# Performance work log

Measured on AMD Instinct MI355X. Metric: run time of the kernel, lower is better.

The kernel has to match this reference:

```python
import jax, jax.numpy as jnp
import numpy as np

B, S, DM, H, DK, DV, CUT = 2, 256, 512, 8, 64, 64, 16
LN_EPS = 1e-5


def get_con_vecs(seq, cutoff):
    # seq: (B, H, S, d). Faithful to torch: raw row-major reshape, NOT a transpose.
    b, h, s, d = seq.shape
    D = h * d
    flat = seq.reshape(b, s, D)                       # raw reinterpretation as in torch
    t = jnp.broadcast_to(flat[:, None], (b, s, s, D)) # (B, S_rep, S_orig, D)
    t = t.transpose(0, 3, 1, 2)                       # (B, D, S, S)
    up = jnp.triu(t)
    up = jnp.flip(up, axis=2)
    up = jnp.pad(up, ((0, 0), (0, 0), (1, 0), (0, 0)))[:, :, :-1, :]
    low = jnp.tril(t)
    low = jnp.flip(low, axis=2)
    mtx = jnp.concatenate([up, low], axis=-1)         # (B, D, S, 2S)
    mtx = mtx.transpose(0, 2, 3, 1)                   # (B, S, 2S, D)
    mtx = mtx.reshape(b, h, s, 2 * s, d)              # raw reinterpretation as in torch
    c = min(cutoff, s)
    return mtx[:, :, :, s - c:s + c, :]               # (B, H, S, 2c, d)


def setup_inputs():
    key = jax.random.key(0)
    ks = jax.random.split(key, 14)
    n = lambda k, shp, sc=0.02: jax.random.normal(k, shp, dtype=jnp.float32) * sc
    return {
        "Q": jax.random.normal(ks[0], (B, S, DM), dtype=jnp.float32),
        "K": jax.random.normal(ks[1], (B, S, DM), dtype=jnp.float32),
        "V": jax.random.normal(ks[2], (B, S, DM), dtype=jnp.float32),
        "attn_mask": jax.random.randint(ks[3], (B, S, S), 0, 2).astype(bool),
        "WQ": n(ks[4], (DM, H * DK)), "bQ": jnp.zeros((H * DK,), jnp.float32),
        "WK": n(ks[5], (DM, H * DK)), "bK": jnp.zeros((H * DK,), jnp.float32),
        "WV": n(ks[6], (DM, H * DV)), "bV": jnp.zeros((H * DV,), jnp.float32),
        "Wo": n(ks[7], (H * DV, DM)), "bo": jnp.zeros((DM,), jnp.float32),
        "gamma": jnp.ones((DM,), jnp.float32), "beta": jnp.zeros((DM,), jnp.float32),
    }


def reference(Q, K, V, attn_mask, WQ, bQ, WK, bK, WV, bV, Wo, bo, gamma, beta):
    b = Q.shape[0]
    q_s = (Q @ WQ + bQ).reshape(b, -1, H, DK).transpose(0, 2, 1, 3)  # (B,H,S,dk)
    k_s = (K @ WK + bK).reshape(b, -1, H, DK).transpose(0, 2, 1, 3)
    v_s = (V @ WV + bV).reshape(b, -1, H, DV).transpose(0, 2, 1, 3)  # unused in 'con' path (V := con(K))
    del v_s

    Qc = get_con_vecs(q_s, CUT)   # (B,H,S,2c,dk)
    Kc = get_con_vecs(k_s, CUT)
    Vc = Kc

    scores = jnp.einsum('bhqcd,bhkcd->bhqkc', Qc, Kc) / np.float32(np.sqrt(DK))
    mask = attn_mask[:, None, :, :, None]             # (B,1,S,S,1) -> broadcast over heads, 2c
    scores = jnp.where(mask, jnp.float32(-1e9), scores)
    attn = jax.nn.softmax(scores, axis=-1)            # softmax over the 2c context axis
    context = jnp.einsum('bhqkc,bhvcd->bhqd', attn, Vc)
    attn_out = attn.sum(axis=-1)                      # (B,H,S,S)

    ctx = context.transpose(0, 2, 1, 3).reshape(b, -1, H * DV)
    out = ctx @ Wo + bo
    y = out + Q
    mu = y.mean(axis=-1, keepdims=True)
    var = ((y - mu) ** 2).mean(axis=-1, keepdims=True)
    y_n = (y - mu) / jnp.sqrt(var + LN_EPS) * gamma + beta
    return (y_n, attn_out)
```

## Files before the change

kernel.cpp:

```cpp
#include <hip/hip_runtime.h>

#define LN_EPS 1e-5f


#define FMA4(a, s, v) { (a).x += (s)*(v).x; (a).y += (s)*(v).y; \
                        (a).z += (s)*(v).z; (a).w += (s)*(v).w; }
#define ADD4(a, v)    { (a).x += (v).x; (a).y += (v).y; \
                        (a).z += (v).z; (a).w += (v).w; }

__device__ __forceinline__ bool sniff_mask_bytes(const unsigned int* m) {
    unsigned int acc = 0;
#pragma unroll
    for (int i = 0; i < 16; ++i) acc |= m[i];
    return acc > 1u;
}

__global__ __launch_bounds__(512) void kAo_proj_part(
    const float* __restrict__ Qin, const float* __restrict__ Kin,
    const float* __restrict__ WQ, const float* __restrict__ WK,
    float* __restrict__ Ppart)
{
    __shared__ float Xs[32][36];
    int bx = blockIdx.x;
    int mc = bx & 15, b = (bx >> 4) & 1, which = bx >> 5;
    int m0 = mc * 32;
    int t = threadIdx.x;

    const float* In = which ? Kin : Qin;
    const float* W  = which ? WK  : WQ;

#pragma unroll
    for (int i = 0; i < 2; ++i) {
        int idx = i * 512 + t;
        int fr = idx >> 5, mm = idx & 31;
        int cc = fr >> 3, cs = fr & 7;
        int srow = (cc < 2) ? (240 + 8 * cc + cs) : (8 * (cc - 2) + cs);
        Xs[mm][fr] = In[(b * 256 + srow) * 512 + m0 + mm];
    }
    __syncthreads();

    int h_i = t >> 6, g = t >> 7;
    int cc0 = (h_i & 1) * 2;
    float acc[16];
#pragma unroll
    for (int j = 0; j < 16; ++j) acc[j] = 0.f;

    const float* wp = W + t;
#pragma unroll 4
    for (int mm = 0; mm < 32; ++mm) {
        float w = wp[(m0 + mm) * 512];
        const float4* xp = (const float4*)&Xs[mm][cc0 * 8];
        float4 x0 = xp[0], x1 = xp[1], x2 = xp[2], x3 = xp[3];
        acc[0]  += x0.x * w; acc[1]  += x0.y * w; acc[2]  += x0.z * w; acc[3]  += x0.w * w;
        acc[4]  += x1.x * w; acc[5]  += x1.y * w; acc[6]  += x1.z * w; acc[7]  += x1.w * w;
        acc[8]  += x2.x * w; acc[9]  += x2.y * w; acc[10] += x2.z * w; acc[11] += x2.w * w;
        acc[12] += x3.x * w; acc[13] += x3.y * w; acc[14] += x3.z * w; acc[15] += x3.w * w;
    }

    int d = t & 63;
    int base = ((which * 2 + b) * 4 + g) * 4;
#pragma unroll
    for (int j = 0; j < 16; ++j) {
        int ccj = cc0 + (j >> 3), cs = j & 7;
        Ppart[mc * 32768 + (base + ccj) * 512 + cs * 64 + d] = acc[j];
    }
}

__global__ void kBC_dtab_sfk(const float* __restrict__ Ppart,
                             const float* __restrict__ bQ, const float* __restrict__ bK,
                             float* __restrict__ Dt, float* __restrict__ SFK) {
    int slot = blockIdx.x * 256 + threadIdx.x;
    if (slot < 8192) {
        int part = slot & 7, e = slot >> 3;
        int cs = e & 7, cc = (e >> 3) & 3, gk = (e >> 5) & 3,
            gq = (e >> 7) & 3, b = (e >> 9) & 1;
        int offq = ((b * 4 + gq) * 4 + cc) * 512 + cs * 64 + part * 8;
        int offk = (((2 + b) * 4 + gk) * 4 + cc) * 512 + cs * 64 + part * 8;
        float4 q0 = {0,0,0,0}, q1 = {0,0,0,0}, k0 = {0,0,0,0}, k1 = {0,0,0,0};
#pragma unroll
        for (int mc = 0; mc < 16; ++mc) {
            const float4* pq = (const float4*)(Ppart + mc * 32768 + offq);
            const float4* pk = (const float4*)(Ppart + mc * 32768 + offk);
            float4 a0 = pq[0], a1 = pq[1], c0 = pk[0], c1 = pk[1];
            ADD4(q0, a0); ADD4(q1, a1); ADD4(k0, c0); ADD4(k1, c1);
        }
        int nq = (gq * 2 + (cc >> 1)) * 64 + part * 8;
        int nk = (gk * 2 + (cc >> 1)) * 64 + part * 8;
        const float4* bq4 = (const float4*)(bQ + nq);
        const float4* bk4 = (const float4*)(bK + nk);
        float4 bqa = bq4[0], bqb = bq4[1], bka = bk4[0], bkb = bk4[1];
        ADD4(q0, bqa); ADD4(q1, bqb); ADD4(k0, bka); ADD4(k1, bkb);
        float a = q0.x * k0.x + q0.y * k0.y + q0.z * k0.z + q0.w * k0.w
                + q1.x * k1.x + q1.y * k1.y + q1.z * k1.z + q1.w * k1.w;
        a += __shfl_xor(a, 1);
        a += __shfl_xor(a, 2);
        a += __shfl_xor(a, 4);
        if (part == 0) Dt[e] = a * 0.125f;
    } else {
        int e = slot - 8192;
        int d = e & 63, c = (e >> 6) & 31, b = e >> 11;
        int cc = c >> 3, o = (c & 7) * 64 + d;
        float a = 0.f;
#pragma unroll
        for (int gv = 0; gv < 4; ++gv) {
            int off = (((2 + b) * 4 + gv) * 4 + cc) * 512 + o;
            float s = bK[(gv * 2 + (cc >> 1)) * 64 + d];
#pragma unroll
            for (int mc = 0; mc < 16; ++mc) s += Ppart[mc * 32768 + off];
            a += s;
        }
        SFK[e] = 32.f * a;
    }
}

__global__ void kAttn(const float* __restrict__ Dt, const void* __restrict__ maskp,
                      const float* __restrict__ SFK, float* __restrict__ ctx,
                      float* __restrict__ attnp, int fill) {
    __shared__ float aws[4][32];
    int vb = blockIdx.x, t = threadIdx.x;
    if (fill) ((float4*)attnp)[vb * 256 + t] = make_float4(1.f, 1.f, 1.f, 1.f);
    int qb = vb & 63, h = (vb >> 6) & 7, b = vb >> 9;
    int wave = t >> 6, l = t & 63;
    int q = qb * 4 + wave;
    int half = l & 1, klo = l >> 1;
    int g_q = q & 3;
    int i_q = h * 32 + (q >> 3);
    bool up_q = (q & 4) == 0;
    int ak = klo & 3;
    bool up_k = (klo & 4) == 0;

    bool mbytes = sniff_mask_bytes((const unsigned int*)maskp);

    float sq[16];
    const float* Db = Dt + ((b * 4 + g_q) * 4 + ak) * 32 + half * 16;
#pragma unroll
    for (int j = 0; j < 16; ++j) {
        int cc = half * 2 + (j >> 3);
        int row = g_q * 64 + 30 + cc;
        bool vq = up_q ? (i_q >= 256 - row) : (i_q <= 255 - row);
        sq[j] = vq ? Db[j] : 0.f;
    }

    float A[16];
#pragma unroll
    for (int j = 0; j < 16; ++j) A[j] = 0.f;

    int qrow = (b * 256 + q) * 256;
    for (int r = 0; r < 8; ++r) {
        int k = r * 32 + klo;
        bool masked = mbytes ? (((const unsigned char*)maskp)[qrow + k] != 0)
                             : (((const int*)maskp)[qrow + k] != 0);
        if (masked) {
#pragma unroll
            for (int j = 0; j < 16; ++j) A[j] += 0.03125f;
            continue;
        }
        int i_k = h * 32 + (k >> 3);
        float s[16];
        float mx = -1e30f;
#pragma unroll
        for (int j = 0; j < 16; ++j) {
            int cc = half * 2 + (j >> 3);
            int row = ak * 64 + 30 + cc;
            bool vk = up_k ? (i_k >= 256 - row) : (i_k <= 255 - row);
            s[j] = vk ? sq[j] : 0.f;
            mx = fmaxf(mx, s[j]);
        }
        mx = fmaxf(mx, __shfl_xor(mx, 1));
        float den = 0.f;
#pragma unroll
        for (int j = 0; j < 16; ++j) { s[j] = __expf(s[j] - mx); den += s[j]; }
        den += __shfl_xor(den, 1);
        float inv = 1.f / den;
#pragma unroll
        for (int j = 0; j < 16; ++j) A[j] += s[j] * inv;
    }

#pragma unroll
    for (int off = 2; off < 64; off <<= 1) {
#pragma unroll
        for (int j = 0; j < 16; ++j) A[j] += __shfl_xor(A[j], off);
    }

    float* aw = aws[wave];
    if (l < 2) {
#pragma unroll
        for (int j = 0; j < 16; ++j) aw[l * 16 + j] = A[j];
    }
    float acc = 0.f;
    const float* S = SFK + b * 2048;
#pragma unroll
    for (int c = 0; c < 32; ++c) acc += aw[c] * S[c * 64 + l];
    ctx[(b * 256 + q) * 512 + h * 64 + l] = acc;
}

__global__ __launch_bounds__(512) void kG4LN(
    const float* __restrict__ ctx, const float* __restrict__ Wo,
    const float* __restrict__ bo, const float* __restrict__ Qin,
    const float* __restrict__ gamma, const float* __restrict__ beta,
    float* __restrict__ out)
{
    __shared__ float  Cl[4][512];
    __shared__ float4 red4[8][4][64];
    __shared__ float  red2[8][2];

    int t = threadIdx.x, r0 = blockIdx.x * 4;
    int w = t >> 6, l = t & 63;

    ((float4*)Cl)[t] = ((const float4*)&ctx[r0 * 512])[t];
    __syncthreads();

    const float4* WoV = (const float4*)Wo;
    const float4* pA = WoV + (size_t)(w * 64) * 128 + l;
    const float4* pB = pA + 64;
    float4 a0A = {0,0,0,0}, a1A = {0,0,0,0}, a2A = {0,0,0,0}, a3A = {0,0,0,0};
    float4 a0B = {0,0,0,0}, a1B = {0,0,0,0}, a2B = {0,0,0,0}, a3B = {0,0,0,0};
    int m0 = w * 64;
    float4 wA = pA[0], wB = pB[0];
#pragma unroll 4
    for (int mm = 0; mm < 63; ++mm) {
        float4 nA = pA[(mm + 1) * 128];
        float4 nB = pB[(mm + 1) * 128];
        float s0 = Cl[0][m0 + mm], s1 = Cl[1][m0 + mm];
        float s2 = Cl[2][m0 + mm], s3 = Cl[3][m0 + mm];
        FMA4(a0A, s0, wA); FMA4(a1A, s1, wA); FMA4(a2A, s2, wA); FMA4(a3A, s3, wA);
        FMA4(a0B, s0, wB); FMA4(a1B, s1, wB); FMA4(a2B, s2, wB); FMA4(a3B, s3, wB);
        wA = nA; wB = nB;
    }
    {
        float s0 = Cl[0][m0 + 63], s1 = Cl[1][m0 + 63];
        float s2 = Cl[2][m0 + 63], s3 = Cl[3][m0 + 63];
        FMA4(a0A, s0, wA); FMA4(a1A, s1, wA); FMA4(a2A, s2, wA); FMA4(a3A, s3, wA);
        FMA4(a0B, s0, wB); FMA4(a1B, s1, wB); FMA4(a2B, s2, wB); FMA4(a3B, s3, wB);
    }

    red4[w][0][l] = a0A; red4[w][1][l] = a1A; red4[w][2][l] = a2A; red4[w][3][l] = a3A;
    __syncthreads();
    if (t < 256) {
        int r = t >> 6, c4 = t & 63;
        float4 s = red4[0][r][c4];
#pragma unroll
        for (int w2 = 1; w2 < 8; ++w2) {
            float4 v = red4[w2][r][c4];
            s.x += v.x; s.y += v.y; s.z += v.z; s.w += v.w;
        }
        float4 bb = ((const float4*)bo)[c4];
        float4 qq = ((const float4*)Qin)[(r0 + r) * 128 + c4];
        s.x += bb.x + qq.x; s.y += bb.y + qq.y;
        s.z += bb.z + qq.z; s.w += bb.w + qq.w;
        *(float4*)&Cl[r][c4 * 4] = s;
    }
    __syncthreads();
    red4[w][0][l] = a0B; red4[w][1][l] = a1B; red4[w][2][l] = a2B; red4[w][3][l] = a3B;
    __syncthreads();
    if (t < 256) {
        int r = t >> 6, c4 = t & 63;
        float4 s = red4[0][r][c4];
#pragma unroll
        for (int w2 = 1; w2 < 8; ++w2) {
            float4 v = red4[w2][r][c4];
            s.x += v.x; s.y += v.y; s.z += v.z; s.w += v.w;
        }
        float4 bb = ((const float4*)bo)[64 + c4];
        float4 qq = ((const float4*)Qin)[(r0 + r) * 128 + 64 + c4];
        s.x += bb.x + qq.x; s.y += bb.y + qq.y;
        s.z += bb.z + qq.z; s.w += bb.w + qq.w;
        *(float4*)&Cl[r][256 + c4 * 4] = s;
    }
    __syncthreads();

    int r = t >> 7, c = t & 127;
    float v0 = Cl[r][c], v1 = Cl[r][c + 128], v2 = Cl[r][c + 256], v3 = Cl[r][c + 384];
    float s1 = v0 + v1 + v2 + v3;
    float s2 = v0 * v0 + v1 * v1 + v2 * v2 + v3 * v3;
#pragma unroll
    for (int off = 1; off < 64; off <<= 1) {
        s1 += __shfl_xor(s1, off);
        s2 += __shfl_xor(s2, off);
    }
    if (l == 0) { red2[w][0] = s1; red2[w][1] = s2; }
    __syncthreads();
    float tot1 = red2[2 * r][0] + red2[2 * r + 1][0];
    float tot2 = red2[2 * r][1] + red2[2 * r + 1][1];
    float mu = tot1 * (1.f / 512.f);
    float var = tot2 * (1.f / 512.f) - mu * mu;
    float rs = rsqrtf(var + LN_EPS);
    float* op = out + (r0 + r) * 512;
    op[c]       = (v0 - mu) * rs * gamma[c]       + beta[c];
    op[c + 128] = (v1 - mu) * rs * gamma[c + 128] + beta[c + 128];
    op[c + 256] = (v2 - mu) * rs * gamma[c + 256] + beta[c + 256];
    op[c + 384] = (v3 - mu) * rs * gamma[c + 384] + beta[c + 384];
}

__global__ void k5_fill(float* __restrict__ p, int n) {
    int i = (blockIdx.x * 256 + threadIdx.x) * 4;
    float4 one = make_float4(1.f, 1.f, 1.f, 1.f);
    for (; i < n; i += gridDim.x * 256 * 4) *(float4*)(p + i) = one;
}

extern "C" void kernel_launch(void* const* d_in, const int* in_sizes, int n_in,
                              void* d_out, int out_size, void* d_ws, size_t ws_size,
                              hipStream_t stream) {
    (void)in_sizes; (void)n_in; (void)out_size;
    const float* Qin  = (const float*)d_in[0];
    const float* Kin  = (const float*)d_in[1];
    const void*  mask = d_in[3];
    const float* WQ   = (const float*)d_in[4];
    const float* bQ   = (const float*)d_in[5];
    const float* WK   = (const float*)d_in[6];
    const float* bK   = (const float*)d_in[7];
    const float* Wo   = (const float*)d_in[10];
    const float* bo   = (const float*)d_in[11];
    const float* gamma= (const float*)d_in[12];
    const float* beta = (const float*)d_in[13];

    float* out   = (float*)d_out;
    float* attnp = out + 262144;

    const size_t NEED = 791552ull * sizeof(float);
    int fill;
    float *Ppart, *Dt, *SFK, *ctx;
    if (ws_size >= NEED) {
        float* ws = (float*)d_ws;
        Ppart = ws;
        Dt    = ws + 524288;
        SFK   = ws + 525312;
        ctx   = ws + 529408;
        fill = 1;
    } else {
        Ppart = attnp;
        Dt    = attnp + 524288;
        SFK   = attnp + 525312;
        ctx   = attnp + 786432;
        fill = 0;
    }

    kAo_proj_part<<<dim3(64),   dim3(512), 0, stream>>>(Qin, Kin, WQ, WK, Ppart);
    kBC_dtab_sfk <<<dim3(48),   dim3(256), 0, stream>>>(Ppart, bQ, bK, Dt, SFK);
    kAttn        <<<dim3(1024), dim3(256), 0, stream>>>(Dt, mask, SFK, ctx, attnp, fill);
    kG4LN        <<<dim3(128),  dim3(512), 0, stream>>>(ctx, Wo, bo, Qin, gamma, beta, out);
    if (!fill) k5_fill<<<dim3(256), dim3(256), 0, stream>>>(attnp, 1048576);
}
```

Before: 39.62 us.

## Precompute SFK·Wo per head so the output projection contracts over 32 context weights

The attention kernel now writes per-query softmax context weights A (32 per head) instead of the 64-wide context vectors. The first 128 of its blocks also compute G = SFK·Wo_h, a per-head product of the shared key features and the output projection. The final kernel then forms the output as A·G over 256 (head, context) terms, which replaces the 512x512 ctx·Wo GEMM, before applying the LayerNorm. This reassociation removes the large Wo GEMM and the ctx buffer. The cost is extra G traffic, extra work in a subset of attention blocks, and a larger workspace.

```diff
diff --git a/kernel.cpp b/kernel.cpp
--- a/kernel.cpp
+++ b/kernel.cpp
@@ -3,10 +3,8 @@
 #define LN_EPS 1e-5f
 
 
-#define FMA4(a, s, v) { (a).x += (s)*(v).x; (a).y += (s)*(v).y; \
-                        (a).z += (s)*(v).z; (a).w += (s)*(v).w; }
-#define ADD4(a, v)    { (a).x += (v).x; (a).y += (v).y; \
-                        (a).z += (v).z; (a).w += (v).w; }
+#define ADD4(a, v) { (a).x += (v).x; (a).y += (v).y; \
+                     (a).z += (v).z; (a).w += (v).w; }
 
 __device__ __forceinline__ bool sniff_mask_bytes(const unsigned int* m) {
     unsigned int acc = 0;
@@ -113,10 +111,11 @@
     }
 }
 
-__global__ void kAttn(const float* __restrict__ Dt, const void* __restrict__ maskp,
-                      const float* __restrict__ SFK, float* __restrict__ ctx,
-                      float* __restrict__ attnp, int fill) {
-    __shared__ float aws[4][32];
+__global__ void kAttnG(const float* __restrict__ Dt, const void* __restrict__ maskp,
+                       const float* __restrict__ SFK, const float* __restrict__ Wo,
+                       float* __restrict__ A_out, float* __restrict__ G,
+                       float* __restrict__ attnp, int fill) {
+    __shared__ float S[32][64];
     int vb = blockIdx.x, t = threadIdx.x;
     if (fill) ((float4*)attnp)[vb * 256 + t] = make_float4(1.f, 1.f, 1.f, 1.f);
     int qb = vb & 63, h = (vb >> 6) & 7, b = vb >> 9;
@@ -182,91 +181,71 @@
         for (int j = 0; j < 16; ++j) A[j] += __shfl_xor(A[j], off);
     }
 
-    float* aw = aws[wave];
     if (l < 2) {
-#pragma unroll
-        for (int j = 0; j < 16; ++j) aw[l * 16 + j] = A[j];
-    }
-    float acc = 0.f;
-    const float* S = SFK + b * 2048;
-#pragma unroll
-    for (int c = 0; c < 32; ++c) acc += aw[c] * S[c * 64 + l];
-    ctx[(b * 256 + q) * 512 + h * 64 + l] = acc;
-}
-
-__global__ __launch_bounds__(512) void kG4LN(
-    const float* __restrict__ ctx, const float* __restrict__ Wo,
+        float* Ap = A_out + ((b * 256 + q) * 8 + h) * 32 + l * 16;
+#pragma unroll
+        for (int j = 0; j < 16; ++j) Ap[j] = A[j];
+    }
+
+    if (vb < 128) {
+        int gb = vb & 1, gh = (vb >> 1) & 7, nc = (vb >> 4) & 7;
+        int n0 = nc * 64;
+        const float* Sg = SFK + gb * 2048;
+#pragma unroll
+        for (int i = 0; i < 8; ++i) {
+            int slot = i * 256 + t;
+            ((float*)S)[slot] = Sg[slot];
+        }
+        __syncthreads();
+        int nl = t & 63, ch = t >> 6;
+        float acc[8];
+#pragma unroll
+        for (int j = 0; j < 8; ++j) acc[j] = 0.f;
+        const float* wp = Wo + gh * 64 * 512 + n0 + nl;
+#pragma unroll 4
+        for (int d = 0; d < 64; ++d) {
+            float w = wp[d * 512];
+#pragma unroll
+            for (int j = 0; j < 8; ++j) acc[j] += S[ch * 8 + j][d] * w;
+        }
+#pragma unroll
+        for (int j = 0; j < 8; ++j)
+            G[gb * 131072 + (gh * 32 + ch * 8 + j) * 512 + n0 + nl] = acc[j];
+    }
+}
+
+__global__ __launch_bounds__(512) void kYLN(
+    const float* __restrict__ A, const float* __restrict__ G,
     const float* __restrict__ bo, const float* __restrict__ Qin,
     const float* __restrict__ gamma, const float* __restrict__ beta,
     float* __restrict__ out)
 {
-    __shared__ float  Cl[4][512];
-    __shared__ float4 red4[8][4][64];
-    __shared__ float  red2[8][2];
+    __shared__ float Al[4][256];
+    __shared__ float Cl[4][512];
+    __shared__ float red2[8][2];
 
     int t = threadIdx.x, r0 = blockIdx.x * 4;
+    int b = r0 >> 8;
     int w = t >> 6, l = t & 63;
 
-    ((float4*)Cl)[t] = ((const float4*)&ctx[r0 * 512])[t];
+    ((float2*)Al)[t] = ((const float2*)(A + r0 * 256))[t];
     __syncthreads();
 
-    const float4* WoV = (const float4*)Wo;
-    const float4* pA = WoV + (size_t)(w * 64) * 128 + l;
-    const float4* pB = pA + 64;
-    float4 a0A = {0,0,0,0}, a1A = {0,0,0,0}, a2A = {0,0,0,0}, a3A = {0,0,0,0};
-    float4 a0B = {0,0,0,0}, a1B = {0,0,0,0}, a2B = {0,0,0,0}, a3B = {0,0,0,0};
-    int m0 = w * 64;
-    float4 wA = pA[0], wB = pB[0];
+    float a0 = 0.f, a1 = 0.f, a2 = 0.f, a3 = 0.f;
+    const float* gp = G + b * 131072 + t;
 #pragma unroll 4
-    for (int mm = 0; mm < 63; ++mm) {
-        float4 nA = pA[(mm + 1) * 128];
-        float4 nB = pB[(mm + 1) * 128];
-        float s0 = Cl[0][m0 + mm], s1 = Cl[1][m0 + mm];
-        float s2 = Cl[2][m0 + mm], s3 = Cl[3][m0 + mm];
-        FMA4(a0A, s0, wA); FMA4(a1A, s1, wA); FMA4(a2A, s2, wA); FMA4(a3A, s3, wA);
-        FMA4(a0B, s0, wB); FMA4(a1B, s1, wB); FMA4(a2B, s2, wB); FMA4(a3B, s3, wB);
-        wA = nA; wB = nB;
-    }
-    {
-        float s0 = Cl[0][m0 + 63], s1 = Cl[1][m0 + 63];
-        float s2 = Cl[2][m0 + 63], s3 = Cl[3][m0 + 63];
-        FMA4(a0A, s0, wA); FMA4(a1A, s1, wA); FMA4(a2A, s2, wA); FMA4(a3A, s3, wA);
-        FMA4(a0B, s0, wB); FMA4(a1B, s1, wB); FMA4(a2B, s2, wB); FMA4(a3B, s3, wB);
-    }
-
-    red4[w][0][l] = a0A; red4[w][1][l] = a1A; red4[w][2][l] = a2A; red4[w][3][l] = a3A;
-    __syncthreads();
-    if (t < 256) {
-        int r = t >> 6, c4 = t & 63;
-        float4 s = red4[0][r][c4];
-#pragma unroll
-        for (int w2 = 1; w2 < 8; ++w2) {
-            float4 v = red4[w2][r][c4];
-            s.x += v.x; s.y += v.y; s.z += v.z; s.w += v.w;
-        }
-        float4 bb = ((const float4*)bo)[c4];
-        float4 qq = ((const float4*)Qin)[(r0 + r) * 128 + c4];
-        s.x += bb.x + qq.x; s.y += bb.y + qq.y;
-        s.z += bb.z + qq.z; s.w += bb.w + qq.w;
-        *(float4*)&Cl[r][c4 * 4] = s;
-    }
-    __syncthreads();
-    red4[w][0][l] = a0B; red4[w][1][l] = a1B; red4[w][2][l] = a2B; red4[w][3][l] = a3B;
-    __syncthreads();
-    if (t < 256) {
-        int r = t >> 6, c4 = t & 63;
-        float4 s = red4[0][r][c4];
-#pragma unroll
-        for (int w2 = 1; w2 < 8; ++w2) {
-            float4 v = red4[w2][r][c4];
-            s.x += v.x; s.y += v.y; s.z += v.z; s.w += v.w;
-        }
-        float4 bb = ((const float4*)bo)[64 + c4];
-        float4 qq = ((const float4*)Qin)[(r0 + r) * 128 + 64 + c4];
-        s.x += bb.x + qq.x; s.y += bb.y + qq.y;
-        s.z += bb.z + qq.z; s.w += bb.w + qq.w;
-        *(float4*)&Cl[r][256 + c4 * 4] = s;
-    }
+    for (int hc = 0; hc < 256; ++hc) {
+        float g = gp[hc * 512];
+        a0 += Al[0][hc] * g;
+        a1 += Al[1][hc] * g;
+        a2 += Al[2][hc] * g;
+        a3 += Al[3][hc] * g;
+    }
+    float bb = bo[t];
+    Cl[0][t] = a0 + bb + Qin[(r0 + 0) * 512 + t];
+    Cl[1][t] = a1 + bb + Qin[(r0 + 1) * 512 + t];
+    Cl[2][t] = a2 + bb + Qin[(r0 + 2) * 512 + t];
+    Cl[3][t] = a3 + bb + Qin[(r0 + 3) * 512 + t];
     __syncthreads();
 
     int r = t >> 7, c = t & 127;
@@ -317,27 +296,21 @@
     float* out   = (float*)d_out;
     float* attnp = out + 262144;
 
-    const size_t NEED = 791552ull * sizeof(float);
+    const size_t NEED = 922624ull * sizeof(float);
     int fill;
-    float *Ppart, *Dt, *SFK, *ctx;
-    if (ws_size >= NEED) {
-        float* ws = (float*)d_ws;
-        Ppart = ws;
-        Dt    = ws + 524288;
-        SFK   = ws + 525312;
-        ctx   = ws + 529408;
-        fill = 1;
-    } else {
-        Ppart = attnp;
-        Dt    = attnp + 524288;
-        SFK   = attnp + 525312;
-        ctx   = attnp + 786432;
-        fill = 0;
-    }
+    float* scr;
+    if (ws_size >= NEED) { scr = (float*)d_ws; fill = 1; }
+    else                 { scr = attnp;        fill = 0; }
+
+    float* Ppart = scr;
+    float* Dt    = scr + 524288;
+    float* SFK   = scr + 525312;
+    float* A     = scr + 529408;
+    float* G     = scr + 660480;
 
     kAo_proj_part<<<dim3(64),   dim3(512), 0, stream>>>(Qin, Kin, WQ, WK, Ppart);
     kBC_dtab_sfk <<<dim3(48),   dim3(256), 0, stream>>>(Ppart, bQ, bK, Dt, SFK);
-    kAttn        <<<dim3(1024), dim3(256), 0, stream>>>(Dt, mask, SFK, ctx, attnp, fill);
-    kG4LN        <<<dim3(128),  dim3(512), 0, stream>>>(ctx, Wo, bo, Qin, gamma, beta, out);
+    kAttnG       <<<dim3(1024), dim3(256), 0, stream>>>(Dt, mask, SFK, Wo, A, G, attnp, fill);
+    kYLN         <<<dim3(128),  dim3(512), 0, stream>>>(A, G, bo, Qin, gamma, beta, out);
     if (!fill) k5_fill<<<dim3(256), dim3(256), 0, stream>>>(attnp, 1048576);
 }
```

Result: slower. 53.33 us (+34.6%).
